# Optimization experiments

Hardware: AMD Instinct MI355X
Metric: run time of the kernel (lower is better)

Reference implementation:

```python
import jax, jax.numpy as jnp
from jax import lax
import numpy as np

V = 30522   # vocab_size
S = 512     # block_size == seq_len
D = 768     # n_hidden
H = 12      # n_heads
L = 12      # n_blocks
F = 3072    # n_mlp_hidden = 4*D
B = 16      # batch
HD = D // H
EPS = 1e-12
SCALE = HD ** (-0.5)


def setup_inputs() -> dict:
    key = jax.random.key(0)
    ks = jax.random.split(key, 16)
    n = lambda k, shape: (0.02 * jax.random.normal(k, shape, dtype=jnp.float32))
    tokens = jax.random.randint(ks[0], (B, S), 0, V)
    return {
        "tokens": tokens,
        # embedding
        "tok_emb": n(ks[1], (V, D)),
        "pos_emb": n(ks[2], (1, S, D)),
        "sent_emb": n(ks[3], (1, 2, D)),
        "emb_ln_w": jnp.ones((D,), jnp.float32),
        "emb_ln_b": jnp.zeros((D,), jnp.float32),
        # stacked per-layer params (torch Linear convention: y = x @ W.T + b)
        "qkv_w": n(ks[4], (L, 3 * D, D)),
        "qkv_b": jnp.zeros((L, 3 * D), jnp.float32),
        "proj_w": n(ks[5], (L, D, D)),
        "proj_b": jnp.zeros((L, D), jnp.float32),
        "ln1_w": jnp.ones((L, D), jnp.float32),
        "ln1_b": jnp.zeros((L, D), jnp.float32),
        "ln2_w": jnp.ones((L, D), jnp.float32),
        "ln2_b": jnp.zeros((L, D), jnp.float32),
        "mlp_w1": n(ks[6], (L, F, D)),
        "mlp_b1": jnp.zeros((L, F), jnp.float32),
        "mlp_w2": n(ks[7], (L, D, F)),
        "mlp_b2": jnp.zeros((L, D), jnp.float32),
        # pooler
        "pool_w": n(ks[8], (D, D)),
        "pool_b": jnp.zeros((D,), jnp.float32),
    }


def _ln(x, w, b):
    mu = x.mean(-1, keepdims=True)
    var = ((x - mu) ** 2).mean(-1, keepdims=True)
    return (x - mu) * lax.rsqrt(var + EPS) * w + b


def reference(tokens, tok_emb, pos_emb, sent_emb, emb_ln_w, emb_ln_b,
              qkv_w, qkv_b, proj_w, proj_b, ln1_w, ln1_b, ln2_w, ln2_b,
              mlp_w1, mlp_b1, mlp_w2, mlp_b2, pool_w, pool_b):
    bs, seq = tokens.shape
    # BERTEmbedding (dropout in eval mode -> identity)
    x = tok_emb[tokens] + pos_emb[:, :seq] + sent_emb[:, :1]
    x = _ln(x, emb_ln_w, emb_ln_b)

    def block(x, p):
        (qw, qb, pw, pb, l1w, l1b, l2w, l2b, w1, b1, w2, b2) = p
        # Attention on raw x (post-norm BERT block)
        qkv = x @ qw.T + qb                              # [B,S,3D]
        q, k, v = [t.reshape(bs, seq, H, HD) for t in jnp.split(qkv, 3, axis=-1)]
        logits = jnp.einsum('bthc,bshc->bhts', q, k) * SCALE
        attn = jax.nn.softmax(logits, axis=-1)
        out = jnp.einsum('bhts,bshc->bthc', attn, v).reshape(bs, seq, D)
        out = out @ pw.T + pb
        x = _ln(x + out, l1w, l1b)
        h = jax.nn.gelu(x @ w1.T + b1, approximate=False)
        x = _ln(x + h @ w2.T + b2, l2w, l2b)
        return x, None

    params = (qkv_w, qkv_b, proj_w, proj_b, ln1_w, ln1_b, ln2_w, ln2_b,
              mlp_w1, mlp_b1, mlp_w2, mlp_b2)
    x, _ = lax.scan(block, x, params)

    # Pooler: first token -> linear -> tanh
    return jnp.tanh(x[:, 0, :] @ pool_w.T + pool_b)
```

## Files before the change

kernel.cpp:

```cpp
#include <hip/hip_runtime.h>
#include <hip/hip_bf16.h>
#include <math.h>

#define B_  16
#define S_  512
#define D_  768
#define H_  12
#define L_  12
#define F_  3072
#define HD_ 64
#define T_  (B_ * S_)
#define SCALE_ 0.125f
#define EPS_ 1e-12f

typedef unsigned short u16;
typedef short  bf16x8 __attribute__((ext_vector_type(8)));
typedef float  f32x4  __attribute__((ext_vector_type(4)));

typedef const void __attribute__((address_space(1))) GVoid;
typedef void       __attribute__((address_space(3))) LVoid;

__device__ __forceinline__ u16 f2bf(float f) {
  unsigned u = __float_as_uint(f);
  u += 0x7fffu + ((u >> 16) & 1u);
  return (u16)(u >> 16);
}

__device__ __forceinline__ void async16(void* lds, const void* g) {
  __builtin_amdgcn_global_load_lds((GVoid*)g, (LVoid*)lds, 16, 0, 0);
}

__global__ void cvt_bf16(const float* __restrict__ in, u16* __restrict__ outp, long n) {
  long i = ((long)blockIdx.x * 256 + threadIdx.x) * 4;
  if (i >= n) return;
  float4 f = *(const float4*)(in + i);
  ushort4 o;
  o.x = f2bf(f.x); o.y = f2bf(f.y); o.z = f2bf(f.z); o.w = f2bf(f.w);
  *(ushort4*)(outp + i) = o;
}

__device__ __forceinline__ float blk_sum(float v) {
  __shared__ float red[4];
  #pragma unroll
  for (int m = 32; m; m >>= 1) v += __shfl_xor(v, m);
  if ((threadIdx.x & 63) == 0) red[threadIdx.x >> 6] = v;
  __syncthreads();
  v = red[0] + red[1] + red[2] + red[3];
  __syncthreads();
  return v;
}

__global__ void embed_ln(const int* __restrict__ tokens, const float* __restrict__ tok_emb,
                         const float* __restrict__ pos_emb, const float* __restrict__ sent_emb,
                         const float* __restrict__ w, const float* __restrict__ bb,
                         float* __restrict__ x32, u16* __restrict__ x16) {
  int t = blockIdx.x;
  int s = t & (S_ - 1);
  int tok = tokens[t];
  float v[3];
  float sum = 0.f;
  #pragma unroll
  for (int i = 0; i < 3; ++i) {
    int c = threadIdx.x + i * 256;
    v[i] = tok_emb[(size_t)tok * D_ + c] + pos_emb[s * D_ + c] + sent_emb[c];
    sum += v[i];
  }
  float mean = blk_sum(sum) * (1.f / D_);
  float var = 0.f;
  #pragma unroll
  for (int i = 0; i < 3; ++i) { float d = v[i] - mean; var += d * d; }
  var = blk_sum(var) * (1.f / D_);
  float rstd = rsqrtf(var + EPS_);
  #pragma unroll
  for (int i = 0; i < 3; ++i) {
    int c = threadIdx.x + i * 256;
    float y = (v[i] - mean) * rstd * w[c] + bb[c];
    x32[(size_t)t * D_ + c] = y;
    x16[(size_t)t * D_ + c] = f2bf(y);
  }
}

__global__ void add_ln(float* __restrict__ x32, u16* __restrict__ x16,
                       const float* __restrict__ y,
                       const float* __restrict__ w, const float* __restrict__ bb) {
  int t = blockIdx.x;
  float v[3];
  float sum = 0.f;
  #pragma unroll
  for (int i = 0; i < 3; ++i) {
    int c = threadIdx.x + i * 256;
    v[i] = x32[(size_t)t * D_ + c] + y[(size_t)t * D_ + c];
    sum += v[i];
  }
  float mean = blk_sum(sum) * (1.f / D_);
  float var = 0.f;
  #pragma unroll
  for (int i = 0; i < 3; ++i) { float d = v[i] - mean; var += d * d; }
  var = blk_sum(var) * (1.f / D_);
  float rstd = rsqrtf(var + EPS_);
  #pragma unroll
  for (int i = 0; i < 3; ++i) {
    int c = threadIdx.x + i * 256;
    float o = (v[i] - mean) * rstd * w[c] + bb[c];
    x32[(size_t)t * D_ + c] = o;
    x16[(size_t)t * D_ + c] = f2bf(o);
  }
}

template<int EPI>
__global__ void gemm_bt(const u16* __restrict__ A, const u16* __restrict__ W,
                        const float* __restrict__ bias, void* __restrict__ outp,
                        int M, int N, int K) {
  __shared__ u16 As[128 * 64];
  __shared__ u16 Bs[128 * 64];
  const int tid  = threadIdx.x;
  const int lane = tid & 63;
  const int wid  = tid >> 6;
  const int m0 = blockIdx.y * 128;
  const int n0 = blockIdx.x * 128;

  const u16* asrc[4]; const u16* bsrc[4];
  u16* adst[4]; u16* bdst[4];
  #pragma unroll
  for (int i = 0; i < 4; ++i) {
    int row  = (i * 4 + wid) * 8 + (lane >> 3);
    int slot = (lane & 7) ^ (row & 7);
    asrc[i] = A + (size_t)(m0 + row) * K + slot * 8;
    bsrc[i] = W + (size_t)(n0 + row) * K + slot * 8;
    adst[i] = &As[(i * 4 + wid) * 512];
    bdst[i] = &Bs[(i * 4 + wid) * 512];
  }

  f32x4 acc[4][4] = {};
  const int wr = wid >> 1, wc = wid & 1;

  for (int kb = 0; kb < K; kb += 64) {
    #pragma unroll
    for (int i = 0; i < 4; ++i) {
      async16(adst[i], asrc[i] + kb);
      async16(bdst[i], bsrc[i] + kb);
    }
    __syncthreads();
    #pragma unroll
    for (int ks = 0; ks < 2; ++ks) {
      bf16x8 af[4], bfr[4];
      #pragma unroll
      for (int m = 0; m < 4; ++m) {
        int row  = wr * 64 + m * 16 + (lane & 15);
        int slot = (ks * 4 + (lane >> 4)) ^ (row & 7);
        af[m] = *(const bf16x8*)&As[row * 64 + slot * 8];
      }
      #pragma unroll
      for (int n = 0; n < 4; ++n) {
        int row  = wc * 64 + n * 16 + (lane & 15);
        int slot = (ks * 4 + (lane >> 4)) ^ (row & 7);
        bfr[n] = *(const bf16x8*)&Bs[row * 64 + slot * 8];
      }
      #pragma unroll
      for (int m = 0; m < 4; ++m)
        #pragma unroll
        for (int n = 0; n < 4; ++n)
          acc[m][n] = __builtin_amdgcn_mfma_f32_16x16x32_bf16(af[m], bfr[n], acc[m][n], 0, 0, 0);
    }
    __syncthreads();
  }

  #pragma unroll
  for (int m = 0; m < 4; ++m) {
    int row = m0 + wr * 64 + m * 16 + ((lane >> 4) << 2);
    #pragma unroll
    for (int n = 0; n < 4; ++n) {
      int col = n0 + wc * 64 + n * 16 + (lane & 15);
      float bv = bias[col];
      #pragma unroll
      for (int r = 0; r < 4; ++r) {
        float v = acc[m][n][r] + bv;
        if (EPI == 1) v = 0.5f * v * (1.0f + erff(v * 0.70710678f));
        if (EPI == 2) ((float*)outp)[(size_t)(row + r) * N + col] = v;
        else          ((u16*) outp)[(size_t)(row + r) * N + col] = f2bf(v);
      }
    }
  }
}

__global__ void attn(const u16* __restrict__ qkv, u16* __restrict__ outp) {
  __shared__ u16 Ks[64 * 64];
  __shared__ u16 Vs[64 * 64];
  __shared__ u16 Ps[4][32 * 64];
  const int tid  = threadIdx.x;
  const int lane = tid & 63;
  const int wid  = tid >> 6;
  const int h = blockIdx.y;
  const int b = blockIdx.z;
  const int q0 = blockIdx.x * 128 + wid * 32;
  const size_t rowbase = (size_t)b * S_;

  bf16x8 qf[2][2];
  #pragma unroll
  for (int mf = 0; mf < 2; ++mf)
    #pragma unroll
    for (int ks = 0; ks < 2; ++ks) {
      size_t r = rowbase + q0 + mf * 16 + (lane & 15);
      int c = h * HD_ + ks * 32 + ((lane >> 4) << 3);
      qf[mf][ks] = *(const bf16x8*)&qkv[r * (3 * D_) + c];
    }

  f32x4 o[2][4] = {};
  float mst[2][4], lst[2][4];
  #pragma unroll
  for (int mf = 0; mf < 2; ++mf)
    #pragma unroll
    for (int r = 0; r < 4; ++r) { mst[mf][r] = -3.0e38f; lst[mf][r] = 0.f; }

  for (int s0 = 0; s0 < S_; s0 += 64) {
    #pragma unroll
    for (int i = 0; i < 2; ++i) {
      int row  = (i * 4 + wid) * 8 + (lane >> 3);
      int slot = lane & 7;
      size_t tok = rowbase + s0 + row;
      async16(&Ks[(i * 4 + wid) * 512],
              &qkv[tok * (3 * D_) + D_     + h * HD_ + (((slot ^ (row & 7)) << 3))]);
      async16(&Vs[(i * 4 + wid) * 512],
              &qkv[tok * (3 * D_) + 2 * D_ + h * HD_ + (slot << 3)]);
    }
    __syncthreads();

    f32x4 sa[2][4] = {};
    #pragma unroll
    for (int ks = 0; ks < 2; ++ks) {
      bf16x8 kf[4];
      #pragma unroll
      for (int n = 0; n < 4; ++n) {
        int row  = n * 16 + (lane & 15);
        int slot = (ks * 4 + (lane >> 4)) ^ (row & 7);
        kf[n] = *(const bf16x8*)&Ks[row * 64 + slot * 8];
      }
      #pragma unroll
      for (int mf = 0; mf < 2; ++mf)
        #pragma unroll
        for (int n = 0; n < 4; ++n)
          sa[mf][n] = __builtin_amdgcn_mfma_f32_16x16x32_bf16(qf[mf][ks], kf[n], sa[mf][n], 0, 0, 0);
    }

    #pragma unroll
    for (int mf = 0; mf < 2; ++mf)
      #pragma unroll
      for (int r = 0; r < 4; ++r) {
        #pragma unroll
        for (int n = 0; n < 4; ++n) sa[mf][n][r] *= SCALE_;
        float mx = fmaxf(fmaxf(sa[mf][0][r], sa[mf][1][r]),
                         fmaxf(sa[mf][2][r], sa[mf][3][r]));
        #pragma unroll
        for (int d = 1; d < 16; d <<= 1) mx = fmaxf(mx, __shfl_xor(mx, d));
        float mnew = fmaxf(mst[mf][r], mx);
        float sc = __expf(mst[mf][r] - mnew);
        float sum = 0.f;
        #pragma unroll
        for (int n = 0; n < 4; ++n) {
          float p = __expf(sa[mf][n][r] - mnew);
          sa[mf][n][r] = p;
          sum += p;
        }
        #pragma unroll
        for (int d = 1; d < 16; d <<= 1) sum += __shfl_xor(sum, d);
        lst[mf][r] = lst[mf][r] * sc + sum;
        mst[mf][r] = mnew;
        #pragma unroll
        for (int n = 0; n < 4; ++n) o[mf][n][r] *= sc;
      }

    #pragma unroll
    for (int mf = 0; mf < 2; ++mf)
      #pragma unroll
      for (int n = 0; n < 4; ++n)
        #pragma unroll
        for (int r = 0; r < 4; ++r) {
          int q = mf * 16 + ((lane >> 4) << 2) + r;
          int s = n * 16 + (lane & 15);
          int slot = (s >> 3) ^ (q & 7);
          Ps[wid][q * 64 + slot * 8 + (s & 7)] = f2bf(sa[mf][n][r]);
        }

    #pragma unroll
    for (int ks = 0; ks < 2; ++ks) {
      bf16x8 pf[2];
      #pragma unroll
      for (int mf = 0; mf < 2; ++mf) {
        int row  = mf * 16 + (lane & 15);
        int slot = (ks * 4 + (lane >> 4)) ^ (row & 7);
        pf[mf] = *(const bf16x8*)&Ps[wid][row * 64 + slot * 8];
      }
      bf16x8 vf[4];
      #pragma unroll
      for (int n = 0; n < 4; ++n) {
        int colv  = n * 16 + (lane & 15);
        int kbase = ks * 32 + ((lane >> 4) << 3);
        #pragma unroll
        for (int j = 0; j < 8; ++j)
          vf[n][j] = (short)Vs[(kbase + j) * 64 + colv];
      }
      #pragma unroll
      for (int mf = 0; mf < 2; ++mf)
        #pragma unroll
        for (int n = 0; n < 4; ++n)
          o[mf][n] = __builtin_amdgcn_mfma_f32_16x16x32_bf16(pf[mf], vf[n], o[mf][n], 0, 0, 0);
    }
    __syncthreads();
  }

  #pragma unroll
  for (int mf = 0; mf < 2; ++mf)
    #pragma unroll
    for (int n = 0; n < 4; ++n)
      #pragma unroll
      for (int r = 0; r < 4; ++r) {
        size_t row = rowbase + q0 + mf * 16 + ((lane >> 4) << 2) + r;
        int col = h * HD_ + n * 16 + (lane & 15);
        outp[row * D_ + col] = f2bf(o[mf][n][r] / lst[mf][r]);
      }
}

__global__ void pooler(const float* __restrict__ x32, const float* __restrict__ pw,
                       const float* __restrict__ pb, float* __restrict__ outp) {
  __shared__ float xr[D_];
  int b = blockIdx.x;
  for (int c = threadIdx.x; c < D_; c += 256) xr[c] = x32[(size_t)b * S_ * D_ + c];
  __syncthreads();
  for (int j = threadIdx.x; j < D_; j += 256) {
    float s = pb[j];
    const float* wr = pw + (size_t)j * D_;
    for (int k = 0; k < D_; ++k) s += xr[k] * wr[k];
    outp[b * D_ + j] = tanhf(s);
  }
}

extern "C" void kernel_launch(void* const* d_in, const int* in_sizes, int n_in,
                              void* d_out, int out_size, void* d_ws, size_t ws_size,
                              hipStream_t stream) {
  (void)in_sizes; (void)n_in; (void)out_size; (void)ws_size;
  const int*   tokens   = (const int*)  d_in[0];
  const float* tok_emb  = (const float*)d_in[1];
  const float* pos_emb  = (const float*)d_in[2];
  const float* sent_emb = (const float*)d_in[3];
  const float* emb_ln_w = (const float*)d_in[4];
  const float* emb_ln_b = (const float*)d_in[5];
  const float* qkv_w    = (const float*)d_in[6];
  const float* qkv_b    = (const float*)d_in[7];
  const float* proj_w   = (const float*)d_in[8];
  const float* proj_b   = (const float*)d_in[9];
  const float* ln1_w    = (const float*)d_in[10];
  const float* ln1_b    = (const float*)d_in[11];
  const float* ln2_w    = (const float*)d_in[12];
  const float* ln2_b    = (const float*)d_in[13];
  const float* mlp_w1   = (const float*)d_in[14];
  const float* mlp_b1   = (const float*)d_in[15];
  const float* mlp_w2   = (const float*)d_in[16];
  const float* mlp_b2   = (const float*)d_in[17];
  const float* pool_w   = (const float*)d_in[18];
  const float* pool_b   = (const float*)d_in[19];

  char* ws = (char*)d_ws;
  size_t off = 0;
  auto alloc = [&](size_t bytes) { void* p = ws + off; off += (bytes + 255) & ~(size_t)255; return p; };
  u16*   WQ  = (u16*)  alloc((size_t)L_ * 3 * D_ * D_ * 2);
  u16*   WP  = (u16*)  alloc((size_t)L_ * D_ * D_ * 2);
  u16*   W1  = (u16*)  alloc((size_t)L_ * F_ * D_ * 2);
  u16*   W2  = (u16*)  alloc((size_t)L_ * D_ * F_ * 2);
  float* Xf  = (float*)alloc((size_t)T_ * D_ * 4);
  u16*   Xb  = (u16*)  alloc((size_t)T_ * D_ * 2);
  u16*   QKV = (u16*)  alloc((size_t)T_ * 3 * D_ * 2);
  u16*   AO  = (u16*)  alloc((size_t)T_ * D_ * 2);
  float* GO  = (float*)alloc((size_t)T_ * D_ * 4);
  u16*   Hb  = (u16*)  alloc((size_t)T_ * F_ * 2);

  {
    long n;
    n = (long)L_ * 3 * D_ * D_;
    cvt_bf16<<<(unsigned)((n / 4 + 255) / 256), 256, 0, stream>>>(qkv_w, WQ, n);
    n = (long)L_ * D_ * D_;
    cvt_bf16<<<(unsigned)((n / 4 + 255) / 256), 256, 0, stream>>>(proj_w, WP, n);
    n = (long)L_ * F_ * D_;
    cvt_bf16<<<(unsigned)((n / 4 + 255) / 256), 256, 0, stream>>>(mlp_w1, W1, n);
    n = (long)L_ * D_ * F_;
    cvt_bf16<<<(unsigned)((n / 4 + 255) / 256), 256, 0, stream>>>(mlp_w2, W2, n);
  }

  embed_ln<<<T_, 256, 0, stream>>>(tokens, tok_emb, pos_emb, sent_emb,
                                   emb_ln_w, emb_ln_b, Xf, Xb);

  for (int l = 0; l < L_; ++l) {
    const u16* wq = WQ + (size_t)l * 3 * D_ * D_;
    const u16* wp = WP + (size_t)l * D_ * D_;
    const u16* w1 = W1 + (size_t)l * F_ * D_;
    const u16* w2 = W2 + (size_t)l * D_ * F_;

    gemm_bt<0><<<dim3(3 * D_ / 128, T_ / 128), 256, 0, stream>>>(
        Xb, wq, qkv_b + (size_t)l * 3 * D_, QKV, T_, 3 * D_, D_);

    attn<<<dim3(S_ / 128, H_, B_), 256, 0, stream>>>(QKV, AO);

    gemm_bt<2><<<dim3(D_ / 128, T_ / 128), 256, 0, stream>>>(
        AO, wp, proj_b + (size_t)l * D_, GO, T_, D_, D_);

    add_ln<<<T_, 256, 0, stream>>>(Xf, Xb, GO, ln1_w + (size_t)l * D_, ln1_b + (size_t)l * D_);

    gemm_bt<1><<<dim3(F_ / 128, T_ / 128), 256, 0, stream>>>(
        Xb, w1, mlp_b1 + (size_t)l * F_, Hb, T_, F_, D_);

    gemm_bt<2><<<dim3(D_ / 128, T_ / 128), 256, 0, stream>>>(
        Hb, w2, mlp_b2 + (size_t)l * D_, GO, T_, D_, F_);

    add_ln<<<T_, 256, 0, stream>>>(Xf, Xb, GO, ln2_w + (size_t)l * D_, ln2_b + (size_t)l * D_);
  }

  pooler<<<B_, 256, 0, stream>>>(Xf, pool_w, pool_b, (float*)d_out);
}
```

Before: 4.476 ms.

## Double-buffer attention K/V, transpose V in LDS, add XCD-aware block remapping

```diff
diff --git a/kernel.cpp b/kernel.cpp
--- a/kernel.cpp
+++ b/kernel.cpp
@@ -39,13 +39,24 @@
   *(ushort4*)(outp + i) = o;
 }
 
-__device__ __forceinline__ float blk_sum(float v) {
+__device__ __forceinline__ float blk_sum4(float v) {
   __shared__ float red[4];
   #pragma unroll
   for (int m = 32; m; m >>= 1) v += __shfl_xor(v, m);
   if ((threadIdx.x & 63) == 0) red[threadIdx.x >> 6] = v;
   __syncthreads();
   v = red[0] + red[1] + red[2] + red[3];
+  __syncthreads();
+  return v;
+}
+
+__device__ __forceinline__ float blk_sum3(float v) {
+  __shared__ float red[3];
+  #pragma unroll
+  for (int m = 32; m; m >>= 1) v += __shfl_xor(v, m);
+  if ((threadIdx.x & 63) == 0) red[threadIdx.x >> 6] = v;
+  __syncthreads();
+  v = red[0] + red[1] + red[2];
   __syncthreads();
   return v;
 }
@@ -65,11 +76,11 @@
     v[i] = tok_emb[(size_t)tok * D_ + c] + pos_emb[s * D_ + c] + sent_emb[c];
     sum += v[i];
   }
-  float mean = blk_sum(sum) * (1.f / D_);
+  float mean = blk_sum4(sum) * (1.f / D_);
   float var = 0.f;
   #pragma unroll
   for (int i = 0; i < 3; ++i) { float d = v[i] - mean; var += d * d; }
-  var = blk_sum(var) * (1.f / D_);
+  var = blk_sum4(var) * (1.f / D_);
   float rstd = rsqrtf(var + EPS_);
   #pragma unroll
   for (int i = 0; i < 3; ++i) {
@@ -84,31 +95,28 @@
                        const float* __restrict__ y,
                        const float* __restrict__ w, const float* __restrict__ bb) {
   int t = blockIdx.x;
-  float v[3];
-  float sum = 0.f;
-  #pragma unroll
-  for (int i = 0; i < 3; ++i) {
-    int c = threadIdx.x + i * 256;
-    v[i] = x32[(size_t)t * D_ + c] + y[(size_t)t * D_ + c];
-    sum += v[i];
-  }
-  float mean = blk_sum(sum) * (1.f / D_);
-  float var = 0.f;
-  #pragma unroll
-  for (int i = 0; i < 3; ++i) { float d = v[i] - mean; var += d * d; }
-  var = blk_sum(var) * (1.f / D_);
+  int c = threadIdx.x * 4;
+  const float4 xv = *(const float4*)&x32[(size_t)t * D_ + c];
+  const float4 yv = *(const float4*)&y  [(size_t)t * D_ + c];
+  float v0 = xv.x + yv.x, v1 = xv.y + yv.y, v2 = xv.z + yv.z, v3 = xv.w + yv.w;
+  float mean = blk_sum3(v0 + v1 + v2 + v3) * (1.f / D_);
+  float d0 = v0 - mean, d1 = v1 - mean, d2 = v2 - mean, d3 = v3 - mean;
+  float var = blk_sum3(d0 * d0 + d1 * d1 + d2 * d2 + d3 * d3) * (1.f / D_);
   float rstd = rsqrtf(var + EPS_);
-  #pragma unroll
-  for (int i = 0; i < 3; ++i) {
-    int c = threadIdx.x + i * 256;
-    float o = (v[i] - mean) * rstd * w[c] + bb[c];
-    x32[(size_t)t * D_ + c] = o;
-    x16[(size_t)t * D_ + c] = f2bf(o);
-  }
+  const float4 wv = *(const float4*)&w[c];
+  const float4 bv = *(const float4*)&bb[c];
+  float o0 = d0 * rstd * wv.x + bv.x;
+  float o1 = d1 * rstd * wv.y + bv.y;
+  float o2 = d2 * rstd * wv.z + bv.z;
+  float o3 = d3 * rstd * wv.w + bv.w;
+  float4 of = {o0, o1, o2, o3};
+  *(float4*)&x32[(size_t)t * D_ + c] = of;
+  ushort4 ob = {f2bf(o0), f2bf(o1), f2bf(o2), f2bf(o3)};
+  *(ushort4*)&x16[(size_t)t * D_ + c] = ob;
 }
 
 template<int EPI>
-__global__ void gemm_bt(const u16* __restrict__ A, const u16* __restrict__ W,
+__global__ __launch_bounds__(256) void gemm_bt(const u16* __restrict__ A, const u16* __restrict__ W,
                         const float* __restrict__ bias, void* __restrict__ outp,
                         int M, int N, int K) {
   __shared__ u16 As[128 * 64];
@@ -116,8 +124,14 @@
   const int tid  = threadIdx.x;
   const int lane = tid & 63;
   const int wid  = tid >> 6;
-  const int m0 = blockIdx.y * 128;
-  const int n0 = blockIdx.x * 128;
+
+  const int gx = gridDim.x;
+  const int nwg = gx * gridDim.y;
+  const int f = blockIdx.y * gx + blockIdx.x;
+  const int q = nwg >> 3, r = nwg & 7, xc = f & 7, pos = f >> 3;
+  const int logical = (xc < r ? xc * (q + 1) : r * (q + 1) + (xc - r) * q) + pos;
+  const int m0 = (logical / gx) * 128;
+  const int n0 = (logical % gx) * 128;
 
   const u16* asrc[4]; const u16* bsrc[4];
   u16* adst[4]; u16* bdst[4];
@@ -173,37 +187,67 @@
       int col = n0 + wc * 64 + n * 16 + (lane & 15);
       float bv = bias[col];
       #pragma unroll
-      for (int r = 0; r < 4; ++r) {
-        float v = acc[m][n][r] + bv;
+      for (int r2 = 0; r2 < 4; ++r2) {
+        float v = acc[m][n][r2] + bv;
         if (EPI == 1) v = 0.5f * v * (1.0f + erff(v * 0.70710678f));
-        if (EPI == 2) ((float*)outp)[(size_t)(row + r) * N + col] = v;
-        else          ((u16*) outp)[(size_t)(row + r) * N + col] = f2bf(v);
-      }
-    }
-  }
-}
-
-__global__ void attn(const u16* __restrict__ qkv, u16* __restrict__ outp) {
-  __shared__ u16 Ks[64 * 64];
-  __shared__ u16 Vs[64 * 64];
+        if (EPI == 2) ((float*)outp)[(size_t)(row + r2) * N + col] = v;
+        else          ((u16*) outp)[(size_t)(row + r2) * N + col] = f2bf(v);
+      }
+    }
+  }
+}
+
+__global__ __launch_bounds__(256) void attn(const u16* __restrict__ qkv, u16* __restrict__ outp) {
+  __shared__ u16 Ks[2][64 * 64];
+  __shared__ u16 Vt[2][64 * 72];
   __shared__ u16 Ps[4][32 * 64];
   const int tid  = threadIdx.x;
   const int lane = tid & 63;
   const int wid  = tid >> 6;
-  const int h = blockIdx.y;
-  const int b = blockIdx.z;
-  const int q0 = blockIdx.x * 128 + wid * 32;
+
+  const int f = blockIdx.x;
+  const int logical = (f & 7) * 96 + (f >> 3);
+  const int qt = logical & 3;
+  const int hb = logical >> 2;
+  const int h  = hb % H_;
+  const int b  = hb / H_;
+  const int q0 = qt * 128 + wid * 32;
   const size_t rowbase = (size_t)b * S_;
+  const int LDQ = 3 * D_;
 
   bf16x8 qf[2][2];
   #pragma unroll
   for (int mf = 0; mf < 2; ++mf)
     #pragma unroll
     for (int ks = 0; ks < 2; ++ks) {
-      size_t r = rowbase + q0 + mf * 16 + (lane & 15);
+      size_t rrow = rowbase + q0 + mf * 16 + (lane & 15);
       int c = h * HD_ + ks * 32 + ((lane >> 4) << 3);
-      qf[mf][ks] = *(const bf16x8*)&qkv[r * (3 * D_) + c];
-    }
+      qf[mf][ks] = *(const bf16x8*)&qkv[rrow * LDQ + c];
+    }
+
+  const int vtok  = tid >> 3;
+  const int vcol0 = (tid & 7) * 8;
+
+  auto stageK = [&](int buf, int s0) {
+    #pragma unroll
+    for (int i = 0; i < 2; ++i) {
+      int chunk = wid * 2 + i;
+      int row   = chunk * 8 + (lane >> 3);
+      int slot  = (lane & 7) ^ (row & 7);
+      async16(&Ks[buf][chunk * 512],
+              &qkv[(rowbase + s0 + row) * LDQ + D_ + h * HD_ + slot * 8]);
+    }
+  };
+  auto loadV = [&](bf16x8* vr, int s0) {
+    #pragma unroll
+    for (int j = 0; j < 2; ++j)
+      vr[j] = *(const bf16x8*)&qkv[(rowbase + s0 + vtok + 32 * j) * LDQ + 2 * D_ + h * HD_ + vcol0];
+  };
+
+  bf16x8 vreg[2][2];
+  stageK(0, 0);
+  loadV(vreg[0], 0);
+  __syncthreads();
 
   f32x4 o[2][4] = {};
   float mst[2][4], lst[2][4];
@@ -212,20 +256,16 @@
     #pragma unroll
     for (int r = 0; r < 4; ++r) { mst[mf][r] = -3.0e38f; lst[mf][r] = 0.f; }
 
-  for (int s0 = 0; s0 < S_; s0 += 64) {
-    #pragma unroll
-    for (int i = 0; i < 2; ++i) {
-      int row  = (i * 4 + wid) * 8 + (lane >> 3);
-      int slot = lane & 7;
-      size_t tok = rowbase + s0 + row;
-      async16(&Ks[(i * 4 + wid) * 512],
-              &qkv[tok * (3 * D_) + D_     + h * HD_ + (((slot ^ (row & 7)) << 3))]);
-      async16(&Vs[(i * 4 + wid) * 512],
-              &qkv[tok * (3 * D_) + 2 * D_ + h * HD_ + (slot << 3)]);
-    }
-    __syncthreads();
+  #pragma unroll
+  for (int t = 0; t < 8; ++t) {
+    const int cur = t & 1, nxt = cur ^ 1;
+    if (t < 7) {
+      stageK(nxt, (t + 1) * 64);
+      loadV(vreg[nxt], (t + 1) * 64);
+    }
 
     f32x4 sa[2][4] = {};
+    __builtin_amdgcn_s_setprio(1);
     #pragma unroll
     for (int ks = 0; ks < 2; ++ks) {
       bf16x8 kf[4];
@@ -233,7 +273,7 @@
       for (int n = 0; n < 4; ++n) {
         int row  = n * 16 + (lane & 15);
         int slot = (ks * 4 + (lane >> 4)) ^ (row & 7);
-        kf[n] = *(const bf16x8*)&Ks[row * 64 + slot * 8];
+        kf[n] = *(const bf16x8*)&Ks[cur][row * 64 + slot * 8];
       }
       #pragma unroll
       for (int mf = 0; mf < 2; ++mf)
@@ -241,6 +281,7 @@
         for (int n = 0; n < 4; ++n)
           sa[mf][n] = __builtin_amdgcn_mfma_f32_16x16x32_bf16(qf[mf][ks], kf[n], sa[mf][n], 0, 0, 0);
     }
+    __builtin_amdgcn_s_setprio(0);
 
     #pragma unroll
     for (int mf = 0; mf < 2; ++mf)
@@ -270,17 +311,31 @@
       }
 
     #pragma unroll
+    for (int j = 0; j < 2; ++j) {
+      int tok = vtok + 32 * j;
+      #pragma unroll
+      for (int e = 0; e < 8; ++e) {
+        int col = vcol0 + e;
+        Vt[cur][col * 72 + (((tok >> 3) ^ (col & 7)) << 3) + (tok & 7)] =
+            (u16)vreg[cur][j][e];
+      }
+    }
+
+    #pragma unroll
     for (int mf = 0; mf < 2; ++mf)
       #pragma unroll
       for (int n = 0; n < 4; ++n)
         #pragma unroll
         for (int r = 0; r < 4; ++r) {
-          int q = mf * 16 + ((lane >> 4) << 2) + r;
-          int s = n * 16 + (lane & 15);
-          int slot = (s >> 3) ^ (q & 7);
-          Ps[wid][q * 64 + slot * 8 + (s & 7)] = f2bf(sa[mf][n][r]);
+          int qq = mf * 16 + ((lane >> 4) << 2) + r;
+          int ss = n * 16 + (lane & 15);
+          int slot = (ss >> 3) ^ (qq & 7);
+          Ps[wid][qq * 64 + slot * 8 + (ss & 7)] = f2bf(sa[mf][n][r]);
         }
 
+    __syncthreads();
+
+    __builtin_amdgcn_s_setprio(1);
     #pragma unroll
     for (int ks = 0; ks < 2; ++ks) {
       bf16x8 pf[2];
@@ -293,11 +348,9 @@
       bf16x8 vf[4];
       #pragma unroll
       for (int n = 0; n < 4; ++n) {
-        int colv  = n * 16 + (lane & 15);
-        int kbase = ks * 32 + ((lane >> 4) << 3);
-        #pragma unroll
-        for (int j = 0; j < 8; ++j)
-          vf[n][j] = (short)Vs[(kbase + j) * 64 + colv];
+        int colv = n * 16 + (lane & 15);
+        int grp  = ks * 4 + (lane >> 4);
+        vf[n] = *(const bf16x8*)&Vt[cur][colv * 72 + ((grp ^ (colv & 7)) << 3)];
       }
       #pragma unroll
       for (int mf = 0; mf < 2; ++mf)
@@ -305,7 +358,7 @@
         for (int n = 0; n < 4; ++n)
           o[mf][n] = __builtin_amdgcn_mfma_f32_16x16x32_bf16(pf[mf], vf[n], o[mf][n], 0, 0, 0);
     }
-    __syncthreads();
+    __builtin_amdgcn_s_setprio(0);
   }
 
   #pragma unroll
@@ -397,12 +450,12 @@
     gemm_bt<0><<<dim3(3 * D_ / 128, T_ / 128), 256, 0, stream>>>(
         Xb, wq, qkv_b + (size_t)l * 3 * D_, QKV, T_, 3 * D_, D_);
 
-    attn<<<dim3(S_ / 128, H_, B_), 256, 0, stream>>>(QKV, AO);
+    attn<<<768, 256, 0, stream>>>(QKV, AO);
 
     gemm_bt<2><<<dim3(D_ / 128, T_ / 128), 256, 0, stream>>>(
         AO, wp, proj_b + (size_t)l * D_, GO, T_, D_, D_);
 
-    add_ln<<<T_, 256, 0, stream>>>(Xf, Xb, GO, ln1_w + (size_t)l * D_, ln1_b + (size_t)l * D_);
+    add_ln<<<T_, 192, 0, stream>>>(Xf, Xb, GO, ln1_w + (size_t)l * D_, ln1_b + (size_t)l * D_);
 
     gemm_bt<1><<<dim3(F_ / 128, T_ / 128), 256, 0, stream>>>(
         Xb, w1, mlp_b1 + (size_t)l * F_, Hb, T_, F_, D_);
@@ -410,7 +463,7 @@
     gemm_bt<2><<<dim3(D_ / 128, T_ / 128), 256, 0, stream>>>(
         Hb, w2, mlp_b2 + (size_t)l * D_, GO, T_, D_, F_);
 
-    add_ln<<<T_, 256, 0, stream>>>(Xf, Xb, GO, ln2_w + (size_t)l * D_, ln2_b + (size_t)l * D_);
+    add_ln<<<T_, 192, 0, stream>>>(Xf, Xb, GO, ln2_w + (size_t)l * D_, ln2_b + (size_t)l * D_);
   }
 
   pooler<<<B_, 256, 0, stream>>>(Xf, pool_w, pool_b, (float*)d_out);
```

After: 4.272 ms. 1.05x faster.
